# Optimization experiments

Measured on AMD Instinct MI355X. Metric: run time of the kernel, lower is better.

## Reference

```python
import jax, jax.numpy as jnp
import numpy as np
import math

D_MODEL = 1024
N_HEADS = 16
D_K = D_MODEL // N_HEADS
B, S = 2, 2048


def setup_inputs() -> dict:
    key = jax.random.key(0)
    ks = jax.random.split(key, 11)
    sc = 1.0 / math.sqrt(D_MODEL)
    inp = {
        'q': jax.random.normal(ks[0], (B, S, D_MODEL), jnp.float32),
        'k': jax.random.normal(ks[1], (B, S, D_MODEL), jnp.float32),
        'v': jax.random.normal(ks[2], (B, S, D_MODEL), jnp.float32),
        'mask': jnp.tril(jnp.ones((S, S), jnp.int32))[None, None],  # [1,1,S,S] causal
        'W_q': jax.random.normal(ks[3], (D_MODEL, D_MODEL), jnp.float32) * sc,
        'b_q': jnp.zeros((D_MODEL,), jnp.float32),
        'W_k': jax.random.normal(ks[4], (D_MODEL, D_MODEL), jnp.float32) * sc,
        'b_k': jnp.zeros((D_MODEL,), jnp.float32),
        'W_v': jax.random.normal(ks[5], (D_MODEL, D_MODEL), jnp.float32) * sc,
        'b_v': jnp.zeros((D_MODEL,), jnp.float32),
        'W_o': jax.random.normal(ks[6], (D_MODEL, D_MODEL), jnp.float32) * sc,
        'b_o': jnp.zeros((D_MODEL,), jnp.float32),
    }
    return inp


def reference(q, k, v, mask, W_q, b_q, W_k, b_k, W_v, b_v, W_o, b_o):
    # Linear projections then split heads: [B,S,D] -> [B,H,S,d_k]
    def split_heads(x):
        b, s, _ = x.shape
        return x.reshape(b, s, N_HEADS, D_K).transpose(0, 2, 1, 3)

    Q = split_heads(q @ W_q + b_q)
    K = split_heads(k @ W_k + b_k)
    V = split_heads(v @ W_v + b_v)

    scores = jnp.einsum('bhqd,bhkd->bhqk', Q, K) / math.sqrt(D_K)
    scores = jnp.where(mask == 0, jnp.float32(-1e9), scores)
    attn = jax.nn.softmax(scores, axis=-1)  # dropout is identity in eval mode
    out = jnp.einsum('bhqk,bhkd->bhqd', attn, V)
    out = out.transpose(0, 2, 1, 3).reshape(q.shape[0], -1, D_MODEL)
    return out @ W_o + b_o
```

## Files before the change

kernel.cpp:

```cpp
#include <hip/hip_runtime.h>
#include <hip/hip_bf16.h>

#define D_MODEL 1024
#define S_LEN   2048
#define BATCH   2
#define NH      16
#define DK      64

typedef __bf16 bf16_t;
typedef __attribute__((ext_vector_type(8))) __bf16 bf16x8;
typedef __attribute__((ext_vector_type(4))) float f32x4;

#if __has_builtin(__builtin_amdgcn_exp2f)
#define EXP2F(x) __builtin_amdgcn_exp2f(x)
#else
#define EXP2F(x) exp2f(x)
#endif

#define Q_SCALE 0.1803368801111204f

#define GLDS16(gp, lp) __builtin_amdgcn_global_load_lds( \
    (const __attribute__((address_space(1))) void*)(gp), \
    (__attribute__((address_space(3))) void*)(lp), 16, 0, 0)

__global__ __launch_bounds__(256) void cvt_qkv(const float* __restrict__ q,
                                               const float* __restrict__ k,
                                               const float* __restrict__ v,
                                               bf16_t* __restrict__ out) {
    const long NELEM = (long)BATCH * S_LEN * D_MODEL;
    const float* src = (blockIdx.y == 0) ? q : (blockIdx.y == 1) ? k : v;
    long i = ((long)blockIdx.x * 256 + threadIdx.x) * 8;
    float4 a = *(const float4*)(src + i);
    float4 b = *(const float4*)(src + i + 4);
    bf16x8 o;
    o[0] = (bf16_t)a.x; o[1] = (bf16_t)a.y; o[2] = (bf16_t)a.z; o[3] = (bf16_t)a.w;
    o[4] = (bf16_t)b.x; o[5] = (bf16_t)b.y; o[6] = (bf16_t)b.z; o[7] = (bf16_t)b.w;
    *(bf16x8*)(out + blockIdx.y * NELEM + i) = o;
}

__global__ void wt_transpose4(const float* __restrict__ Wq, const float* __restrict__ Wk,
                              const float* __restrict__ Wv, const float* __restrict__ Wo,
                              bf16_t* __restrict__ WqkvT, bf16_t* __restrict__ WoT) {
    __shared__ float t[32][33];
    const float* in = (blockIdx.z == 0) ? Wq : (blockIdx.z == 1) ? Wk
                    : (blockIdx.z == 2) ? Wv : Wo;
    bf16_t* out = (blockIdx.z < 3) ? (WqkvT + (long)blockIdx.z * D_MODEL * D_MODEL) : WoT;
    int tx = threadIdx.x, ty = threadIdx.y;
    int gx = blockIdx.x * 32, gy = blockIdx.y * 32;
#pragma unroll
    for (int i = 0; i < 32; i += 8)
        t[ty + i][tx] = in[(gy + ty + i) * D_MODEL + gx + tx];
    __syncthreads();
#pragma unroll
    for (int i = 0; i < 32; i += 8)
        out[(gx + ty + i) * D_MODEL + gy + tx] = (bf16_t)t[tx][ty + i];
}

__global__ void v_transpose(const bf16_t* __restrict__ in, bf16_t* __restrict__ out) {
    __shared__ bf16_t t[32][33];
    int tx = threadIdx.x, ty = threadIdx.y;
    int bh = blockIdx.z;
    int s0 = blockIdx.x * 32, d0 = blockIdx.y * 32;
    const bf16_t* ip = in + (long)bh * S_LEN * DK;
    bf16_t* op = out + (long)bh * DK * S_LEN;
#pragma unroll
    for (int i = 0; i < 32; i += 8)
        t[ty + i][tx] = ip[(long)(s0 + ty + i) * DK + d0 + tx];
    __syncthreads();
#pragma unroll
    for (int i = 0; i < 32; i += 8)
        op[(long)(d0 + ty + i) * S_LEN + s0 + tx] = t[tx][ty + i];
}

#define BM 128
#define BN 128
#define BKT 64

__device__ __forceinline__ void swizzle_xy(int bx, int by, int& n0, int& m0) {
    int lin = by * 8 + bx;
    n0 = (lin >> 5) * BN;
    m0 = (lin & 31) * BM;
}

__device__ __forceinline__ void stage_swz(const bf16_t* __restrict__ G, int row0,
                                          int k0, bf16_t* __restrict__ Ls, int tid) {
#pragma unroll
    for (int it = 0; it < 4; ++it) {
        int g = it * 256 + tid;
        int row = g >> 3;
        int c = (g & 7) ^ (row & 7);
        GLDS16(&G[(long)(row0 + row) * D_MODEL + k0 + c * 8],
               &Ls[(it * 256 + (tid & ~63)) * 8]);
    }
}

__device__ __forceinline__ bf16x8 frag_swz(const bf16_t* __restrict__ Ls, int row, int cg) {
    return *(const bf16x8*)(&Ls[(row * 8 + (cg ^ (row & 7))) * 8]);
}

__global__ __launch_bounds__(256) void gemm_qkv(
    const bf16_t* __restrict__ qkvb, const bf16_t* __restrict__ WqkvT,
    const float* __restrict__ bq, const float* __restrict__ bk, const float* __restrict__ bv,
    bf16_t* __restrict__ Qw, bf16_t* __restrict__ Kw, bf16_t* __restrict__ Vw)
{
    __shared__ __align__(16) bf16_t As[BM * BKT];
    __shared__ __align__(16) bf16_t Bs[BN * BKT];
    const int z = blockIdx.z;
    const bf16_t* A  = qkvb + (long)z * BATCH * S_LEN * D_MODEL;
    const bf16_t* BT = WqkvT + (long)z * D_MODEL * D_MODEL;
    const float* bias = (z == 0) ? bq : (z == 1) ? bk : bv;
    bf16_t* Cb = (z == 0) ? Qw : (z == 1) ? Kw : Vw;
    const float oscale = (z == 0) ? Q_SCALE : 1.0f;

    const int tid  = threadIdx.x;
    const int wave = tid >> 6, lane = tid & 63;
    const int lrow = lane & 15, kgrp = lane >> 4;
    const int wm = (wave >> 1) * 64, wn = (wave & 1) * 64;
    int m0, n0;
    swizzle_xy(blockIdx.x, blockIdx.y, n0, m0);

    f32x4 acc[4][4] = {};

    for (int k0 = 0; k0 < D_MODEL; k0 += BKT) {
        stage_swz(A, m0, k0, As, tid);
        stage_swz(BT, n0, k0, Bs, tid);
        __syncthreads();
#pragma unroll
        for (int kk = 0; kk < 2; ++kk) {
            bf16x8 af[4], bfr[4];
#pragma unroll
            for (int mi = 0; mi < 4; ++mi)
                af[mi] = frag_swz(As, wm + mi * 16 + lrow, kk * 4 + kgrp);
#pragma unroll
            for (int ni = 0; ni < 4; ++ni)
                bfr[ni] = frag_swz(Bs, wn + ni * 16 + lrow, kk * 4 + kgrp);
#pragma unroll
            for (int mi = 0; mi < 4; ++mi)
#pragma unroll
                for (int ni = 0; ni < 4; ++ni)
                    acc[mi][ni] = __builtin_amdgcn_mfma_f32_16x16x32_bf16(af[mi], bfr[ni], acc[mi][ni], 0, 0, 0);
        }
        __syncthreads();
    }

#pragma unroll
    for (int mi = 0; mi < 4; ++mi)
#pragma unroll
        for (int ni = 0; ni < 4; ++ni) {
            int col = n0 + wn + ni * 16 + lrow;
            float bvf = bias[col];
#pragma unroll
            for (int r = 0; r < 4; ++r) {
                int row = m0 + wm + mi * 16 + kgrp * 4 + r;
                float vv = (acc[mi][ni][r] + bvf) * oscale;
                int b = row >> 11, s = row & (S_LEN - 1);
                int h = col >> 6, d = col & (DK - 1);
                Cb[(((long)(b * NH + h) * S_LEN + s) * DK) + d] = (bf16_t)vv;
            }
        }
}

__global__ __launch_bounds__(256) void gemm_out(
    const bf16_t* __restrict__ A, const bf16_t* __restrict__ BT,
    const float* __restrict__ bias, float* __restrict__ Cf)
{
    __shared__ __align__(16) bf16_t As[BM * BKT];
    __shared__ __align__(16) bf16_t Bs[BN * BKT];
    const int tid  = threadIdx.x;
    const int wave = tid >> 6, lane = tid & 63;
    const int lrow = lane & 15, kgrp = lane >> 4;
    const int wm = (wave >> 1) * 64, wn = (wave & 1) * 64;
    int m0, n0;
    swizzle_xy(blockIdx.x, blockIdx.y, n0, m0);

    f32x4 acc[4][4] = {};

    for (int k0 = 0; k0 < D_MODEL; k0 += BKT) {
        stage_swz(A, m0, k0, As, tid);
        stage_swz(BT, n0, k0, Bs, tid);
        __syncthreads();
#pragma unroll
        for (int kk = 0; kk < 2; ++kk) {
            bf16x8 af[4], bfr[4];
#pragma unroll
            for (int mi = 0; mi < 4; ++mi)
                af[mi] = frag_swz(As, wm + mi * 16 + lrow, kk * 4 + kgrp);
#pragma unroll
            for (int ni = 0; ni < 4; ++ni)
                bfr[ni] = frag_swz(Bs, wn + ni * 16 + lrow, kk * 4 + kgrp);
#pragma unroll
            for (int mi = 0; mi < 4; ++mi)
#pragma unroll
                for (int ni = 0; ni < 4; ++ni)
                    acc[mi][ni] = __builtin_amdgcn_mfma_f32_16x16x32_bf16(af[mi], bfr[ni], acc[mi][ni], 0, 0, 0);
        }
        __syncthreads();
    }

#pragma unroll
    for (int mi = 0; mi < 4; ++mi)
#pragma unroll
        for (int ni = 0; ni < 4; ++ni) {
            int col = n0 + wn + ni * 16 + lrow;
            float bvf = bias[col];
#pragma unroll
            for (int r = 0; r < 4; ++r) {
                int row = m0 + wm + mi * 16 + kgrp * 4 + r;
                Cf[(long)row * D_MODEL + col] = acc[mi][ni][r] + bvf;
            }
        }
}

__device__ __forceinline__ void attn_one_qtile(
    int qi, int bh, int wave, int lrow, int kgrp,
    int r0, int c0, int r1,
    const bf16_t* __restrict__ Qh, const bf16_t* __restrict__ Kh,
    const bf16_t* __restrict__ Vth, bf16_t* __restrict__ O,
    bf16_t* __restrict__ Ks, bf16_t* __restrict__ Vs, bf16_t* __restrict__ Pw)
{
    const int q0 = qi * 64;
    const int qrow = q0 + wave * 16;

    bf16x8 qf[2];
#pragma unroll
    for (int kk = 0; kk < 2; ++kk)
        qf[kk] = *(const bf16x8*)(&Qh[(qrow + lrow) * DK + kk * 32 + kgrp * 8]);

    f32x4 acc[4] = {};
    float lsum[4] = {0.f, 0.f, 0.f, 0.f};

    const int nt = qi + 1;

    uint4 kpre0 = *(const uint4*)(&Kh[(long)r0 * DK + c0]);
    uint4 kpre1 = *(const uint4*)(&Kh[(long)r1 * DK + c0]);
    uint4 vpre0 = *(const uint4*)(&Vth[(long)r0 * S_LEN + c0]);
    uint4 vpre1 = *(const uint4*)(&Vth[(long)r1 * S_LEN + c0]);

    for (int t = 0; t < nt; ++t) {
        __syncthreads();
        *(uint4*)(&Ks[r0 * 72 + c0]) = kpre0;
        *(uint4*)(&Ks[r1 * 72 + c0]) = kpre1;
        *(uint4*)(&Vs[r0 * 72 + c0]) = vpre0;
        *(uint4*)(&Vs[r1 * 72 + c0]) = vpre1;
        if (t + 1 < nt) {
            const int j0n = (t + 1) * 64;
            kpre0 = *(const uint4*)(&Kh[(long)(j0n + r0) * DK + c0]);
            kpre1 = *(const uint4*)(&Kh[(long)(j0n + r1) * DK + c0]);
            vpre0 = *(const uint4*)(&Vth[(long)r0 * S_LEN + j0n + c0]);
            vpre1 = *(const uint4*)(&Vth[(long)r1 * S_LEN + j0n + c0]);
        }
        __syncthreads();

        const int j0 = t * 64;

        f32x4 sc[4] = {};
#pragma unroll
        for (int kk = 0; kk < 2; ++kk)
#pragma unroll
            for (int ni = 0; ni < 4; ++ni) {
                bf16x8 kf = *(const bf16x8*)(&Ks[(ni * 16 + lrow) * 72 + kk * 32 + kgrp * 8]);
                sc[ni] = __builtin_amdgcn_mfma_f32_16x16x32_bf16(qf[kk], kf, sc[ni], 0, 0, 0);
            }

        const bool needmask = (j0 + 63 > qrow);
        if (needmask) {
#pragma unroll
            for (int r = 0; r < 4; ++r) {
                int row = qrow + kgrp * 4 + r;
#pragma unroll
                for (int ni = 0; ni < 4; ++ni) {
                    int colj = j0 + ni * 16 + lrow;
                    float pv = EXP2F(sc[ni][r]);
                    if (colj > row) pv = 0.f;
                    lsum[r] += pv;
                    Pw[(kgrp * 4 + r) * 72 + ni * 16 + lrow] = (bf16_t)pv;
                }
            }
        } else {
#pragma unroll
            for (int r = 0; r < 4; ++r)
#pragma unroll
                for (int ni = 0; ni < 4; ++ni) {
                    float pv = EXP2F(sc[ni][r]);
                    lsum[r] += pv;
                    Pw[(kgrp * 4 + r) * 72 + ni * 16 + lrow] = (bf16_t)pv;
                }
        }

#pragma unroll
        for (int kk = 0; kk < 2; ++kk) {
            bf16x8 pf = *(const bf16x8*)(&Pw[lrow * 72 + kk * 32 + kgrp * 8]);
#pragma unroll
            for (int di = 0; di < 4; ++di) {
                bf16x8 vf = *(const bf16x8*)(&Vs[(di * 16 + lrow) * 72 + kk * 32 + kgrp * 8]);
                acc[di] = __builtin_amdgcn_mfma_f32_16x16x32_bf16(pf, vf, acc[di], 0, 0, 0);
            }
        }
    }

#pragma unroll
    for (int r = 0; r < 4; ++r)
#pragma unroll
        for (int off = 1; off < 16; off <<= 1)
            lsum[r] += __shfl_xor(lsum[r], off);

    const int b = bh >> 4, h = bh & (NH - 1);
#pragma unroll
    for (int r = 0; r < 4; ++r) {
        int s = qrow + kgrp * 4 + r;
        float inv = 1.f / lsum[r];
#pragma unroll
        for (int di = 0; di < 4; ++di) {
            int d = di * 16 + lrow;
            O[((long)(b * S_LEN + s)) * D_MODEL + h * DK + d] = (bf16_t)(acc[di][r] * inv);
        }
    }
}

__global__ __launch_bounds__(256, 2) void attn_kernel(
    const bf16_t* __restrict__ Q, const bf16_t* __restrict__ K,
    const bf16_t* __restrict__ Vt, bf16_t* __restrict__ O)
{
    __shared__ __align__(16) bf16_t Ks[64 * 72];
    __shared__ __align__(16) bf16_t Vs[64 * 72];
    __shared__ __align__(16) bf16_t Ps[4][16 * 72];

    const int bh = blockIdx.y;
    const int p  = blockIdx.x;
    const int tid = threadIdx.x, wave = tid >> 6, lane = tid & 63;
    const int lrow = lane & 15, kgrp = lane >> 4;

    const bf16_t* Qh  = Q  + (long)bh * S_LEN * DK;
    const bf16_t* Kh  = K  + (long)bh * S_LEN * DK;
    const bf16_t* Vth = Vt + (long)bh * DK * S_LEN;

    const int f0 = tid * 8;
    const int r0 = f0 >> 6, c0 = f0 & 63;
    const int r1 = (f0 + 2048) >> 6;

    attn_one_qtile(31 - p, bh, wave, lrow, kgrp, r0, c0, r1,
                   Qh, Kh, Vth, O, Ks, Vs, Ps[wave]);
    attn_one_qtile(p, bh, wave, lrow, kgrp, r0, c0, r1,
                   Qh, Kh, Vth, O, Ks, Vs, Ps[wave]);
}

extern "C" void kernel_launch(void* const* d_in, const int* in_sizes, int n_in,
                              void* d_out, int out_size, void* d_ws, size_t ws_size,
                              hipStream_t stream) {
    const float* q  = (const float*)d_in[0];
    const float* k  = (const float*)d_in[1];
    const float* v  = (const float*)d_in[2];
    const float* Wq = (const float*)d_in[4];
    const float* bq = (const float*)d_in[5];
    const float* Wk = (const float*)d_in[6];
    const float* bk = (const float*)d_in[7];
    const float* Wv = (const float*)d_in[8];
    const float* bv = (const float*)d_in[9];
    const float* Wo = (const float*)d_in[10];
    const float* bo = (const float*)d_in[11];

    char* ws = (char*)d_ws;
    const size_t Mi = 1024 * 1024;
    bf16_t* WqkvT = (bf16_t*)(ws);
    bf16_t* WoT   = (bf16_t*)(ws + 6 * Mi);
    bf16_t* Qw    = (bf16_t*)(ws + 8 * Mi);
    bf16_t* Kw    = (bf16_t*)(ws + 16 * Mi);
    bf16_t* Vw    = (bf16_t*)(ws + 24 * Mi);
    bf16_t* qkvb  = (bf16_t*)(ws + 32 * Mi);
    bf16_t* Vtw   = (bf16_t*)(ws + 32 * Mi);
    bf16_t* Aw    = (bf16_t*)(ws + 24 * Mi);

    const long NELEM = (long)BATCH * S_LEN * D_MODEL;
    cvt_qkv<<<dim3((int)(NELEM / 2048), 3), 256, 0, stream>>>(q, k, v, qkvb);

    dim3 tb(32, 8);
    wt_transpose4<<<dim3(D_MODEL / 32, D_MODEL / 32, 4), tb, 0, stream>>>(
        Wq, Wk, Wv, Wo, WqkvT, WoT);

    gemm_qkv<<<dim3(D_MODEL / BN, (BATCH * S_LEN) / BM, 3), 256, 0, stream>>>(
        qkvb, WqkvT, bq, bk, bv, Qw, Kw, Vw);

    v_transpose<<<dim3(S_LEN / 32, DK / 32, BATCH * NH), tb, 0, stream>>>(Vw, Vtw);

    attn_kernel<<<dim3(16, BATCH * NH), 256, 0, stream>>>(Qw, Kw, Vtw, Aw);

    gemm_out<<<dim3(D_MODEL / BN, (BATCH * S_LEN) / BM), 256, 0, stream>>>(
        Aw, WoT, bo, (float*)d_out);
}
```

Measured before the change: 239.8 us.

## Process paired causal query tiles in one K/V sweep sharing loaded tiles

The attention kernel used to run two passes over K/V, one for the long query tile and one for the short one. It now makes a single pass, computing both query tiles against each shared K/V tile while that tile is in LDS. The short tile's work is predicated off once its causal range ends. This halves the global K/V loads and sync iterations for the short tile and adds ILP between the two MFMA chains, at the cost of more registers (two accumulator sets) and extra LDS for a second P buffer, which may hurt occupancy under launch_bounds(256,2).

```diff
diff --git a/kernel.cpp b/kernel.cpp
--- a/kernel.cpp
+++ b/kernel.cpp
@@ -211,25 +211,41 @@
         }
 }
 
-__device__ __forceinline__ void attn_one_qtile(
-    int qi, int bh, int wave, int lrow, int kgrp,
-    int r0, int c0, int r1,
-    const bf16_t* __restrict__ Qh, const bf16_t* __restrict__ Kh,
-    const bf16_t* __restrict__ Vth, bf16_t* __restrict__ O,
-    bf16_t* __restrict__ Ks, bf16_t* __restrict__ Vs, bf16_t* __restrict__ Pw)
+__global__ __launch_bounds__(256, 2) void attn_kernel(
+    const bf16_t* __restrict__ Q, const bf16_t* __restrict__ K,
+    const bf16_t* __restrict__ Vt, bf16_t* __restrict__ O)
 {
-    const int q0 = qi * 64;
-    const int qrow = q0 + wave * 16;
-
-    bf16x8 qf[2];
-#pragma unroll
-    for (int kk = 0; kk < 2; ++kk)
-        qf[kk] = *(const bf16x8*)(&Qh[(qrow + lrow) * DK + kk * 32 + kgrp * 8]);
-
-    f32x4 acc[4] = {};
-    float lsum[4] = {0.f, 0.f, 0.f, 0.f};
-
-    const int nt = qi + 1;
+    __shared__ __align__(16) bf16_t Ks[64 * 72];
+    __shared__ __align__(16) bf16_t Vs[64 * 72];
+    __shared__ __align__(16) bf16_t Ps[2][4][16 * 72];
+
+    const int bh = blockIdx.y;
+    const int p  = blockIdx.x;
+    const int qiL = 31 - p, qiH = p;
+    const int tid = threadIdx.x, wave = tid >> 6, lane = tid & 63;
+    const int lrow = lane & 15, kgrp = lane >> 4;
+    const int qrowL = qiL * 64 + wave * 16;
+    const int qrowH = qiH * 64 + wave * 16;
+
+    const bf16_t* Qh  = Q  + (long)bh * S_LEN * DK;
+    const bf16_t* Kh  = K  + (long)bh * S_LEN * DK;
+    const bf16_t* Vth = Vt + (long)bh * DK * S_LEN;
+
+    const int f0 = tid * 8;
+    const int r0 = f0 >> 6, c0 = f0 & 63;
+    const int r1 = (f0 + 2048) >> 6;
+
+    bf16x8 qfL[2], qfH[2];
+#pragma unroll
+    for (int kk = 0; kk < 2; ++kk) {
+        qfL[kk] = *(const bf16x8*)(&Qh[(qrowL + lrow) * DK + kk * 32 + kgrp * 8]);
+        qfH[kk] = *(const bf16x8*)(&Qh[(qrowH + lrow) * DK + kk * 32 + kgrp * 8]);
+    }
+
+    f32x4 accL[4] = {}, accH[4] = {};
+    float lsumL[4] = {0.f, 0.f, 0.f, 0.f}, lsumH[4] = {0.f, 0.f, 0.f, 0.f};
+
+    const int nt = qiL + 1;
 
     uint4 kpre0 = *(const uint4*)(&Kh[(long)r0 * DK + c0]);
     uint4 kpre1 = *(const uint4*)(&Kh[(long)r1 * DK + c0]);
@@ -252,48 +268,83 @@
         __syncthreads();
 
         const int j0 = t * 64;
-
-        f32x4 sc[4] = {};
+        const bool doH = (t <= qiH);
+
+        f32x4 scL[4] = {}, scH[4] = {};
 #pragma unroll
         for (int kk = 0; kk < 2; ++kk)
 #pragma unroll
             for (int ni = 0; ni < 4; ++ni) {
                 bf16x8 kf = *(const bf16x8*)(&Ks[(ni * 16 + lrow) * 72 + kk * 32 + kgrp * 8]);
-                sc[ni] = __builtin_amdgcn_mfma_f32_16x16x32_bf16(qf[kk], kf, sc[ni], 0, 0, 0);
-            }
-
-        const bool needmask = (j0 + 63 > qrow);
-        if (needmask) {
-#pragma unroll
-            for (int r = 0; r < 4; ++r) {
-                int row = qrow + kgrp * 4 + r;
-#pragma unroll
-                for (int ni = 0; ni < 4; ++ni) {
-                    int colj = j0 + ni * 16 + lrow;
-                    float pv = EXP2F(sc[ni][r]);
-                    if (colj > row) pv = 0.f;
-                    lsum[r] += pv;
-                    Pw[(kgrp * 4 + r) * 72 + ni * 16 + lrow] = (bf16_t)pv;
+                scL[ni] = __builtin_amdgcn_mfma_f32_16x16x32_bf16(qfL[kk], kf, scL[ni], 0, 0, 0);
+                if (doH)
+                    scH[ni] = __builtin_amdgcn_mfma_f32_16x16x32_bf16(qfH[kk], kf, scH[ni], 0, 0, 0);
+            }
+
+        {
+            const bool needmask = (j0 + 63 > qrowL);
+            if (needmask) {
+#pragma unroll
+                for (int r = 0; r < 4; ++r) {
+                    int row = qrowL + kgrp * 4 + r;
+#pragma unroll
+                    for (int ni = 0; ni < 4; ++ni) {
+                        int colj = j0 + ni * 16 + lrow;
+                        float pv = EXP2F(scL[ni][r]);
+                        if (colj > row) pv = 0.f;
+                        lsumL[r] += pv;
+                        Ps[0][wave][(kgrp * 4 + r) * 72 + ni * 16 + lrow] = (bf16_t)pv;
+                    }
                 }
-            }
-        } else {
-#pragma unroll
-            for (int r = 0; r < 4; ++r)
-#pragma unroll
-                for (int ni = 0; ni < 4; ++ni) {
-                    float pv = EXP2F(sc[ni][r]);
-                    lsum[r] += pv;
-                    Pw[(kgrp * 4 + r) * 72 + ni * 16 + lrow] = (bf16_t)pv;
+            } else {
+#pragma unroll
+                for (int r = 0; r < 4; ++r)
+#pragma unroll
+                    for (int ni = 0; ni < 4; ++ni) {
+                        float pv = EXP2F(scL[ni][r]);
+                        lsumL[r] += pv;
+                        Ps[0][wave][(kgrp * 4 + r) * 72 + ni * 16 + lrow] = (bf16_t)pv;
+                    }
+            }
+        }
+        if (doH) {
+            const bool needmask = (j0 + 63 > qrowH);
+            if (needmask) {
+#pragma unroll
+                for (int r = 0; r < 4; ++r) {
+                    int row = qrowH + kgrp * 4 + r;
+#pragma unroll
+                    for (int ni = 0; ni < 4; ++ni) {
+                        int colj = j0 + ni * 16 + lrow;
+                        float pv = EXP2F(scH[ni][r]);
+                        if (colj > row) pv = 0.f;
+                        lsumH[r] += pv;
+                        Ps[1][wave][(kgrp * 4 + r) * 72 + ni * 16 + lrow] = (bf16_t)pv;
+                    }
                 }
+            } else {
+#pragma unroll
+                for (int r = 0; r < 4; ++r)
+#pragma unroll
+                    for (int ni = 0; ni < 4; ++ni) {
+                        float pv = EXP2F(scH[ni][r]);
+                        lsumH[r] += pv;
+                        Ps[1][wave][(kgrp * 4 + r) * 72 + ni * 16 + lrow] = (bf16_t)pv;
+                    }
+            }
         }
 
 #pragma unroll
         for (int kk = 0; kk < 2; ++kk) {
-            bf16x8 pf = *(const bf16x8*)(&Pw[lrow * 72 + kk * 32 + kgrp * 8]);
+            bf16x8 pfL = *(const bf16x8*)(&Ps[0][wave][lrow * 72 + kk * 32 + kgrp * 8]);
+            bf16x8 pfH;
+            if (doH) pfH = *(const bf16x8*)(&Ps[1][wave][lrow * 72 + kk * 32 + kgrp * 8]);
 #pragma unroll
             for (int di = 0; di < 4; ++di) {
                 bf16x8 vf = *(const bf16x8*)(&Vs[(di * 16 + lrow) * 72 + kk * 32 + kgrp * 8]);
-                acc[di] = __builtin_amdgcn_mfma_f32_16x16x32_bf16(pf, vf, acc[di], 0, 0, 0);
+                accL[di] = __builtin_amdgcn_mfma_f32_16x16x32_bf16(pfL, vf, accL[di], 0, 0, 0);
+                if (doH)
+                    accH[di] = __builtin_amdgcn_mfma_f32_16x16x32_bf16(pfH, vf, accH[di], 0, 0, 0);
             }
         }
     }
@@ -301,47 +352,23 @@
 #pragma unroll
     for (int r = 0; r < 4; ++r)
 #pragma unroll
-        for (int off = 1; off < 16; off <<= 1)
-            lsum[r] += __shfl_xor(lsum[r], off);
+        for (int off = 1; off < 16; off <<= 1) {
+            lsumL[r] += __shfl_xor(lsumL[r], off);
+            lsumH[r] += __shfl_xor(lsumH[r], off);
+        }
 
     const int b = bh >> 4, h = bh & (NH - 1);
 #pragma unroll
     for (int r = 0; r < 4; ++r) {
-        int s = qrow + kgrp * 4 + r;
-        float inv = 1.f / lsum[r];
+        int sL = qrowL + kgrp * 4 + r, sH = qrowH + kgrp * 4 + r;
+        float invL = 1.f / lsumL[r], invH = 1.f / lsumH[r];
 #pragma unroll
         for (int di = 0; di < 4; ++di) {
             int d = di * 16 + lrow;
-            O[((long)(b * S_LEN + s)) * D_MODEL + h * DK + d] = (bf16_t)(acc[di][r] * inv);
-        }
-    }
-}
-
-__global__ __launch_bounds__(256, 2) void attn_kernel(
-    const bf16_t* __restrict__ Q, const bf16_t* __restrict__ K,
-    const bf16_t* __restrict__ Vt, bf16_t* __restrict__ O)
-{
-    __shared__ __align__(16) bf16_t Ks[64 * 72];
-    __shared__ __align__(16) bf16_t Vs[64 * 72];
-    __shared__ __align__(16) bf16_t Ps[4][16 * 72];
-
-    const int bh = blockIdx.y;
-    const int p  = blockIdx.x;
-    const int tid = threadIdx.x, wave = tid >> 6, lane = tid & 63;
-    const int lrow = lane & 15, kgrp = lane >> 4;
-
-    const bf16_t* Qh  = Q  + (long)bh * S_LEN * DK;
-    const bf16_t* Kh  = K  + (long)bh * S_LEN * DK;
-    const bf16_t* Vth = Vt + (long)bh * DK * S_LEN;
-
-    const int f0 = tid * 8;
-    const int r0 = f0 >> 6, c0 = f0 & 63;
-    const int r1 = (f0 + 2048) >> 6;
-
-    attn_one_qtile(31 - p, bh, wave, lrow, kgrp, r0, c0, r1,
-                   Qh, Kh, Vth, O, Ks, Vs, Ps[wave]);
-    attn_one_qtile(p, bh, wave, lrow, kgrp, r0, c0, r1,
-                   Qh, Kh, Vth, O, Ks, Vs, Ps[wave]);
+            O[((long)(b * S_LEN + sL)) * D_MODEL + h * DK + d] = (bf16_t)(accL[di][r] * invL);
+            O[((long)(b * S_LEN + sH)) * D_MODEL + h * DK + d] = (bf16_t)(accH[di][r] * invH);
+        }
+    }
 }
 
 extern "C" void kernel_launch(void* const* d_in, const int* in_sizes, int n_in,
```

Measured after the change: 246.7 us. 2.9% more time.
